# Kernel optimization log

Hardware: AMD Instinct MI355X
Metric: run time of the kernel (lower is better)

The kernel has to match this reference:

```python
import jax, jax.numpy as jnp
import numpy as np

M = 200000   # number of lane candidates
N = 5000     # number of obstacles
NUM_NODE = 150
FEAT = 4


def setup_inputs() -> dict:
    key = jax.random.key(0)
    k1, k2, k3 = jax.random.split(key, 3)
    lane_features = jax.random.normal(k1, (M, NUM_NODE, FEAT), dtype=jnp.float32)
    obs_pos = jax.random.normal(k2, (N, 2), dtype=jnp.float32)
    same_obs_mask = jnp.sort(jax.random.randint(k3, (M, 1), 0, N), axis=0)
    return {"lane_features": lane_features, "obs_pos": obs_pos,
            "same_obs_mask": same_obs_mask}


def reference(lane_features, obs_pos, same_obs_mask):
    lf = lane_features.astype(jnp.float32)          # (M, 150, 4)
    m = lf.shape[0]
    ar = jnp.arange(m)

    # BroadcastObstaclesToLanes: the serial masked-write loop is exactly a gather.
    rep = obs_pos[same_obs_mask[:, 0]].astype(jnp.float32)   # (M, 2)

    # FindClosestNodeFromLineToPoint: interior nodes [1:-1], xy only.
    nodes = lf[:, 1:-1, :2]                          # (M, 148, 2)
    dists = jnp.sum((nodes - rep[:, None, :]) ** 2, axis=-1)  # (M, 148)
    min_idx = jnp.argmin(dists, axis=1) + 1          # (M,), in [1, 148]

    # FindClosestLineSegmentFromLineToPoint (note: distances use all 4 feats,
    # faithfully matching line_nodes[..., :] in the original).
    min_node = lf[ar, min_idx]                       # (M, 4)
    node_prev = lf[ar, min_idx - 1]
    node_next = lf[ar, min_idx + 1]
    dist_prev = jnp.sum((node_prev - min_node) ** 2, axis=1)
    dist_next = jnp.sum((node_next - min_node) ** 2, axis=1)
    min_idx_2nd = jnp.where(dist_next < dist_prev, min_idx + 1, min_idx - 1)
    idx_before = jnp.minimum(min_idx, min_idx_2nd)
    idx_after = jnp.maximum(min_idx, min_idx_2nd)

    # PointToLineProjection on the xy of the chosen segment endpoints.
    seg_s = lf[ar, idx_before, :2]                   # (M, 2)
    seg_e = lf[ar, idx_after, :2]                    # (M, 2)
    line_vec = seg_e - seg_s
    mag = jnp.sqrt(jnp.sum(line_vec ** 2, axis=1, keepdims=True))
    unit = line_vec / mag
    proj_mag = jnp.sum((rep - seg_s) * unit, axis=1, keepdims=True)
    proj_pt = seg_s + proj_mag * unit                # (M, 2)

    indices = jnp.stack([idx_before, idx_after], axis=1)  # (M, 2)
    return proj_pt, indices, rep
```

## Files before the change

kernel.cpp:

```cpp
#include <hip/hip_runtime.h>
#include <math.h>

static constexpr int M_ROWS   = 200000;
static constexpr int NUM_NODE = 150;
static constexpr int ROW_F    = NUM_NODE * 4;
static constexpr int BLOCKS   = 2048;
static constexpr int WPB      = 4;
static constexpr int TOTAL_WAVES = BLOCKS * WPB;

__global__ __launch_bounds__(256, 6) void obstacle_to_lane_kernel(
    const float* __restrict__ lf,
    const float* __restrict__ obs_pos,
    const int*   __restrict__ mask,
    float*       __restrict__ out)
{
    const int wave = threadIdx.x >> 6;
    const int lane = threadIdx.x & 63;
    const int wid  = blockIdx.x * WPB + wave;

    const int base = M_ROWS / TOTAL_WAVES;
    const int rem  = M_ROWS % TOTAL_WAVES;
    const int m0   = wid * base + (wid < rem ? wid : rem);
    const int m1   = m0 + base + (wid < rem ? 1 : 0);

    const int  j0   = lane;
    const int  j1   = lane + 64;
    const int  j2c  = (lane + 128 <= NUM_NODE - 1) ? (lane + 128) : (NUM_NODE - 1);
    const bool amin0 = (j0 >= 1);
    const bool amin2 = (lane + 128 <= NUM_NODE - 2);

    const float* row = lf + (size_t)m0 * ROW_F;

    float4 c0 = *reinterpret_cast<const float4*>(row + 4 * j0);
    float4 c1 = *reinterpret_cast<const float4*>(row + 4 * j1);
    float4 c2 = *reinterpret_cast<const float4*>(row + 4 * j2c);
    int obs0 = mask[m0];
    float rx = obs_pos[2 * obs0];
    float ry = obs_pos[2 * obs0 + 1];

    for (int m = m0; m < m1; ++m) {
        float4 n0, n1, n2;
        float nrx, nry;
        const bool has_next = (m + 1 < m1);
        if (has_next) {
            const float* nrow = row + ROW_F;
            n0 = *reinterpret_cast<const float4*>(nrow + 4 * j0);
            n1 = *reinterpret_cast<const float4*>(nrow + 4 * j1);
            n2 = *reinterpret_cast<const float4*>(nrow + 4 * j2c);
            const int nobs = mask[m + 1];
            nrx = obs_pos[2 * nobs];
            nry = obs_pos[2 * nobs + 1];
        }

        float best_d = INFINITY;
        int   best_j = 1 << 30;
        {
            float dx = __fsub_rn(c0.x, rx), dy = __fsub_rn(c0.y, ry);
            float d  = __fadd_rn(__fmul_rn(dx, dx), __fmul_rn(dy, dy));
            if (amin0 && d < best_d) { best_d = d; best_j = j0; }
            dx = __fsub_rn(c1.x, rx); dy = __fsub_rn(c1.y, ry);
            d  = __fadd_rn(__fmul_rn(dx, dx), __fmul_rn(dy, dy));
            if (d < best_d) { best_d = d; best_j = j1; }
            dx = __fsub_rn(c2.x, rx); dy = __fsub_rn(c2.y, ry);
            d  = __fadd_rn(__fmul_rn(dx, dx), __fmul_rn(dy, dy));
            if (amin2 && d < best_d) { best_d = d; best_j = lane + 128; }
        }
        #pragma unroll
        for (int off = 32; off > 0; off >>= 1) {
            const float od = __shfl_down(best_d, off, 64);
            const int   oj = __shfl_down(best_j, off, 64);
            if (od < best_d || (od == best_d && oj < best_j)) { best_d = od; best_j = oj; }
        }
        const int min_idx = __shfl(best_j, 0, 64);

        auto pick = [&](int q) -> float4 {
            const int sl = q & 63;
            const int rr = q >> 6;
            const float4 s = (rr == 0) ? c0 : ((rr == 1) ? c1 : c2);
            float4 r;
            r.x = __shfl(s.x, sl, 64);
            r.y = __shfl(s.y, sl, 64);
            r.z = __shfl(s.z, sl, 64);
            r.w = __shfl(s.w, sl, 64);
            return r;
        };
        const float4 na = pick(min_idx - 1);
        const float4 nc = pick(min_idx);
        const float4 nb = pick(min_idx + 1);

        float t, s;
        t = __fsub_rn(na.x, nc.x); s = __fmul_rn(t, t);
        t = __fsub_rn(na.y, nc.y); s = __fadd_rn(s, __fmul_rn(t, t));
        t = __fsub_rn(na.z, nc.z); s = __fadd_rn(s, __fmul_rn(t, t));
        t = __fsub_rn(na.w, nc.w); s = __fadd_rn(s, __fmul_rn(t, t));
        const float dist_prev = s;
        t = __fsub_rn(nb.x, nc.x); s = __fmul_rn(t, t);
        t = __fsub_rn(nb.y, nc.y); s = __fadd_rn(s, __fmul_rn(t, t));
        t = __fsub_rn(nb.z, nc.z); s = __fadd_rn(s, __fmul_rn(t, t));
        t = __fsub_rn(nb.w, nc.w); s = __fadd_rn(s, __fmul_rn(t, t));
        const float dist_next = s;

        float sx, sy, ex, ey;
        int ib;
        if (dist_next < dist_prev) {
            ib = min_idx;     sx = nc.x; sy = nc.y; ex = nb.x; ey = nb.y;
        } else {
            ib = min_idx - 1; sx = na.x; sy = na.y; ex = nc.x; ey = nc.y;
        }

        const float lvx = __fsub_rn(ex, sx);
        const float lvy = __fsub_rn(ey, sy);
        const float mag = __fsqrt_rn(__fadd_rn(__fmul_rn(lvx, lvx), __fmul_rn(lvy, lvy)));
        const float ux  = __fdiv_rn(lvx, mag);
        const float uy  = __fdiv_rn(lvy, mag);
        const float pm  = __fadd_rn(__fmul_rn(__fsub_rn(rx, sx), ux),
                                    __fmul_rn(__fsub_rn(ry, sy), uy));
        const float px  = __fadd_rn(sx, __fmul_rn(pm, ux));
        const float py  = __fadd_rn(sy, __fmul_rn(pm, uy));

        if (lane < 3) {
            float2 v;
            size_t off;
            if (lane == 0) {
                v = make_float2(px, py);
                off = 2 * (size_t)m;
            } else if (lane == 1) {
                v = make_float2((float)ib, (float)(ib + 1));
                off = 2 * (size_t)M_ROWS + 2 * (size_t)m;
            } else {
                v = make_float2(rx, ry);
                off = 4 * (size_t)M_ROWS + 2 * (size_t)m;
            }
            *reinterpret_cast<float2*>(out + off) = v;
        }

        if (has_next) {
            row += ROW_F;
            c0 = n0; c1 = n1; c2 = n2;
            rx = nrx; ry = nry;
        }
    }
}

extern "C" void kernel_launch(void* const* d_in, const int* in_sizes, int n_in,
                              void* d_out, int out_size, void* d_ws, size_t ws_size,
                              hipStream_t stream) {
    const float* lf      = (const float*)d_in[0];
    const float* obs_pos = (const float*)d_in[1];
    const int*   mask    = (const int*)d_in[2];
    float*       out     = (float*)d_out;

    hipLaunchKernelGGL(obstacle_to_lane_kernel, dim3(BLOCKS), dim3(256), 0, stream,
                       lf, obs_pos, mask, out);
}
```

Before: 649.1 us.

## Replace persistent row loop with one-shot waves processing two rows each

Drops the persistent grid, where each wave looped over about 24 rows with a one-row software prefetch. The new launch uses M/8 blocks, and each wave handles exactly two rows, issuing all six row loads up front and interleaving the two argmin reductions and shuffles. The goal is more memory-level parallelism and the removal of loop and prefetch overhead, relying on the hardware scheduler to hide latency across many waves. The trade-off is many more blocks to launch, and it relies on M being divisible by 8.

```diff
diff --git a/kernel.cpp b/kernel.cpp
--- a/kernel.cpp
+++ b/kernel.cpp
@@ -4,11 +4,9 @@
 static constexpr int M_ROWS   = 200000;
 static constexpr int NUM_NODE = 150;
 static constexpr int ROW_F    = NUM_NODE * 4;
-static constexpr int BLOCKS   = 2048;
-static constexpr int WPB      = 4;
-static constexpr int TOTAL_WAVES = BLOCKS * WPB;
+static constexpr int ROWS_PER_BLOCK = 8;
 
-__global__ __launch_bounds__(256, 6) void obstacle_to_lane_kernel(
+__global__ __launch_bounds__(256) void obstacle_to_lane_kernel(
     const float* __restrict__ lf,
     const float* __restrict__ obs_pos,
     const int*   __restrict__ mask,
@@ -16,78 +14,82 @@
 {
     const int wave = threadIdx.x >> 6;
     const int lane = threadIdx.x & 63;
-    const int wid  = blockIdx.x * WPB + wave;
+    const int mA = blockIdx.x * ROWS_PER_BLOCK + wave * 2;
+    const int mB = mA + 1;
 
-    const int base = M_ROWS / TOTAL_WAVES;
-    const int rem  = M_ROWS % TOTAL_WAVES;
-    const int m0   = wid * base + (wid < rem ? wid : rem);
-    const int m1   = m0 + base + (wid < rem ? 1 : 0);
-
-    const int  j0   = lane;
-    const int  j1   = lane + 64;
-    const int  j2c  = (lane + 128 <= NUM_NODE - 1) ? (lane + 128) : (NUM_NODE - 1);
+    const int  j0 = lane;
+    const int  j1 = lane + 64;
+    const int  j2c = (lane + 128 < NUM_NODE) ? (lane + 128) : (NUM_NODE - 1);
     const bool amin0 = (j0 >= 1);
     const bool amin2 = (lane + 128 <= NUM_NODE - 2);
 
-    const float* row = lf + (size_t)m0 * ROW_F;
+    const float* rowA = lf + (size_t)mA * ROW_F;
+    const float* rowB = rowA + ROW_F;
 
-    float4 c0 = *reinterpret_cast<const float4*>(row + 4 * j0);
-    float4 c1 = *reinterpret_cast<const float4*>(row + 4 * j1);
-    float4 c2 = *reinterpret_cast<const float4*>(row + 4 * j2c);
-    int obs0 = mask[m0];
-    float rx = obs_pos[2 * obs0];
-    float ry = obs_pos[2 * obs0 + 1];
+    const int oA = mask[mA];
+    const int oB = mask[mB];
+    const float4 a0 = *reinterpret_cast<const float4*>(rowA + 4 * j0);
+    const float4 a1 = *reinterpret_cast<const float4*>(rowA + 4 * j1);
+    const float4 a2 = *reinterpret_cast<const float4*>(rowA + 4 * j2c);
+    const float4 b0 = *reinterpret_cast<const float4*>(rowB + 4 * j0);
+    const float4 b1 = *reinterpret_cast<const float4*>(rowB + 4 * j1);
+    const float4 b2 = *reinterpret_cast<const float4*>(rowB + 4 * j2c);
+    const float rxA = obs_pos[2 * oA], ryA = obs_pos[2 * oA + 1];
+    const float rxB = obs_pos[2 * oB], ryB = obs_pos[2 * oB + 1];
 
-    for (int m = m0; m < m1; ++m) {
-        float4 n0, n1, n2;
-        float nrx, nry;
-        const bool has_next = (m + 1 < m1);
-        if (has_next) {
-            const float* nrow = row + ROW_F;
-            n0 = *reinterpret_cast<const float4*>(nrow + 4 * j0);
-            n1 = *reinterpret_cast<const float4*>(nrow + 4 * j1);
-            n2 = *reinterpret_cast<const float4*>(nrow + 4 * j2c);
-            const int nobs = mask[m + 1];
-            nrx = obs_pos[2 * nobs];
-            nry = obs_pos[2 * nobs + 1];
-        }
+    float dA = INFINITY; int jA = 1 << 30;
+    float dB = INFINITY; int jB = 1 << 30;
+    {
+        float dx, dy, d;
+        dx = __fsub_rn(a0.x, rxA); dy = __fsub_rn(a0.y, ryA);
+        d  = __fadd_rn(__fmul_rn(dx, dx), __fmul_rn(dy, dy));
+        if (amin0 && d < dA) { dA = d; jA = j0; }
+        dx = __fsub_rn(b0.x, rxB); dy = __fsub_rn(b0.y, ryB);
+        d  = __fadd_rn(__fmul_rn(dx, dx), __fmul_rn(dy, dy));
+        if (amin0 && d < dB) { dB = d; jB = j0; }
 
-        float best_d = INFINITY;
-        int   best_j = 1 << 30;
-        {
-            float dx = __fsub_rn(c0.x, rx), dy = __fsub_rn(c0.y, ry);
-            float d  = __fadd_rn(__fmul_rn(dx, dx), __fmul_rn(dy, dy));
-            if (amin0 && d < best_d) { best_d = d; best_j = j0; }
-            dx = __fsub_rn(c1.x, rx); dy = __fsub_rn(c1.y, ry);
-            d  = __fadd_rn(__fmul_rn(dx, dx), __fmul_rn(dy, dy));
-            if (d < best_d) { best_d = d; best_j = j1; }
-            dx = __fsub_rn(c2.x, rx); dy = __fsub_rn(c2.y, ry);
-            d  = __fadd_rn(__fmul_rn(dx, dx), __fmul_rn(dy, dy));
-            if (amin2 && d < best_d) { best_d = d; best_j = lane + 128; }
-        }
-        #pragma unroll
-        for (int off = 32; off > 0; off >>= 1) {
-            const float od = __shfl_down(best_d, off, 64);
-            const int   oj = __shfl_down(best_j, off, 64);
-            if (od < best_d || (od == best_d && oj < best_j)) { best_d = od; best_j = oj; }
-        }
-        const int min_idx = __shfl(best_j, 0, 64);
+        dx = __fsub_rn(a1.x, rxA); dy = __fsub_rn(a1.y, ryA);
+        d  = __fadd_rn(__fmul_rn(dx, dx), __fmul_rn(dy, dy));
+        if (d < dA) { dA = d; jA = j1; }
+        dx = __fsub_rn(b1.x, rxB); dy = __fsub_rn(b1.y, ryB);
+        d  = __fadd_rn(__fmul_rn(dx, dx), __fmul_rn(dy, dy));
+        if (d < dB) { dB = d; jB = j1; }
 
-        auto pick = [&](int q) -> float4 {
-            const int sl = q & 63;
-            const int rr = q >> 6;
-            const float4 s = (rr == 0) ? c0 : ((rr == 1) ? c1 : c2);
-            float4 r;
-            r.x = __shfl(s.x, sl, 64);
-            r.y = __shfl(s.y, sl, 64);
-            r.z = __shfl(s.z, sl, 64);
-            r.w = __shfl(s.w, sl, 64);
-            return r;
-        };
-        const float4 na = pick(min_idx - 1);
-        const float4 nc = pick(min_idx);
-        const float4 nb = pick(min_idx + 1);
+        dx = __fsub_rn(a2.x, rxA); dy = __fsub_rn(a2.y, ryA);
+        d  = __fadd_rn(__fmul_rn(dx, dx), __fmul_rn(dy, dy));
+        if (amin2 && d < dA) { dA = d; jA = lane + 128; }
+        dx = __fsub_rn(b2.x, rxB); dy = __fsub_rn(b2.y, ryB);
+        d  = __fadd_rn(__fmul_rn(dx, dx), __fmul_rn(dy, dy));
+        if (amin2 && d < dB) { dB = d; jB = lane + 128; }
+    }
 
+    #pragma unroll
+    for (int off = 32; off > 0; off >>= 1) {
+        const float odA = __shfl_down(dA, off, 64);
+        const int   ojA = __shfl_down(jA, off, 64);
+        const float odB = __shfl_down(dB, off, 64);
+        const int   ojB = __shfl_down(jB, off, 64);
+        if (odA < dA || (odA == dA && ojA < jA)) { dA = odA; jA = ojA; }
+        if (odB < dB || (odB == dB && ojB < jB)) { dB = odB; jB = ojB; }
+    }
+    const int min_idxA = __shfl(jA, 0, 64);
+    const int min_idxB = __shfl(jB, 0, 64);
+
+    auto pick = [&](const float4& s0, const float4& s1, const float4& s2, int q) -> float4 {
+        const int sl = q & 63;
+        const int rr = q >> 6;
+        const float4 s = (rr == 0) ? s0 : ((rr == 1) ? s1 : s2);
+        float4 r;
+        r.x = __shfl(s.x, sl, 64);
+        r.y = __shfl(s.y, sl, 64);
+        r.z = __shfl(s.z, sl, 64);
+        r.w = __shfl(s.w, sl, 64);
+        return r;
+    };
+
+    auto epilogue = [&](const float4& na, const float4& nc, const float4& nb,
+                        int min_idx, float rx, float ry,
+                        float& px, float& py, int& ib) {
         float t, s;
         t = __fsub_rn(na.x, nc.x); s = __fmul_rn(t, t);
         t = __fsub_rn(na.y, nc.y); s = __fadd_rn(s, __fmul_rn(t, t));
@@ -101,7 +103,6 @@
         const float dist_next = s;
 
         float sx, sy, ex, ey;
-        int ib;
         if (dist_next < dist_prev) {
             ib = min_idx;     sx = nc.x; sy = nc.y; ex = nb.x; ey = nb.y;
         } else {
@@ -115,30 +116,39 @@
         const float uy  = __fdiv_rn(lvy, mag);
         const float pm  = __fadd_rn(__fmul_rn(__fsub_rn(rx, sx), ux),
                                     __fmul_rn(__fsub_rn(ry, sy), uy));
-        const float px  = __fadd_rn(sx, __fmul_rn(pm, ux));
-        const float py  = __fadd_rn(sy, __fmul_rn(pm, uy));
+        px = __fadd_rn(sx, __fmul_rn(pm, ux));
+        py = __fadd_rn(sy, __fmul_rn(pm, uy));
+    };
 
-        if (lane < 3) {
-            float2 v;
-            size_t off;
-            if (lane == 0) {
-                v = make_float2(px, py);
-                off = 2 * (size_t)m;
-            } else if (lane == 1) {
-                v = make_float2((float)ib, (float)(ib + 1));
-                off = 2 * (size_t)M_ROWS + 2 * (size_t)m;
-            } else {
-                v = make_float2(rx, ry);
-                off = 4 * (size_t)M_ROWS + 2 * (size_t)m;
-            }
-            *reinterpret_cast<float2*>(out + off) = v;
+    const float4 naA = pick(a0, a1, a2, min_idxA - 1);
+    const float4 ncA = pick(a0, a1, a2, min_idxA);
+    const float4 nbA = pick(a0, a1, a2, min_idxA + 1);
+    const float4 naB = pick(b0, b1, b2, min_idxB - 1);
+    const float4 ncB = pick(b0, b1, b2, min_idxB);
+    const float4 nbB = pick(b0, b1, b2, min_idxB + 1);
+
+    float pxA, pyA, pxB, pyB;
+    int ibA, ibB;
+    epilogue(naA, ncA, nbA, min_idxA, rxA, ryA, pxA, pyA, ibA);
+    epilogue(naB, ncB, nbB, min_idxB, rxB, ryB, pxB, pyB, ibB);
+
+    if (lane < 6) {
+        const bool isB  = lane >= 3;
+        const int  m    = isB ? mB : mA;
+        const int  slot = isB ? lane - 3 : lane;
+        float2 v; size_t off;
+        if (slot == 0) {
+            v = make_float2(isB ? pxB : pxA, isB ? pyB : pyA);
+            off = 2 * (size_t)m;
+        } else if (slot == 1) {
+            const int ib = isB ? ibB : ibA;
+            v = make_float2((float)ib, (float)(ib + 1));
+            off = 2 * (size_t)M_ROWS + 2 * (size_t)m;
+        } else {
+            v = make_float2(isB ? rxB : rxA, isB ? ryB : ryA);
+            off = 4 * (size_t)M_ROWS + 2 * (size_t)m;
         }
-
-        if (has_next) {
-            row += ROW_F;
-            c0 = n0; c1 = n1; c2 = n2;
-            rx = nrx; ry = nry;
-        }
+        *reinterpret_cast<float2*>(out + off) = v;
     }
 }
 
@@ -150,6 +160,7 @@
     const int*   mask    = (const int*)d_in[2];
     float*       out     = (float*)d_out;
 
-    hipLaunchKernelGGL(obstacle_to_lane_kernel, dim3(BLOCKS), dim3(256), 0, stream,
+    const int grid = M_ROWS / ROWS_PER_BLOCK;
+    hipLaunchKernelGGL(obstacle_to_lane_kernel, dim3(grid), dim3(256), 0, stream,
                        lf, obs_pos, mask, out);
 }
```

Result: faster. 611.7 us (-5.8%).
